# Optimization experiments

Measured on AMD Instinct MI355X. Metric: run time of the kernel, lower is better.

The kernel has to match this reference:

```python
import jax, jax.numpy as jnp
import numpy as np

B, S, D = 2, 2048, 2048
QH, KVH, HD = 32, 8, 64
GRP = QH // KVH  # GQA group size = 4


def setup_inputs() -> dict:
    key = jax.random.key(0)
    ks = jax.random.split(key, 9)
    x = jax.random.normal(ks[0], (B, S, D), jnp.float32)
    # RoPE angle table: [S, HD//2] -> stacked (cos, sin) -> [S, HD//2, 2]
    inv_freq = 1.0 / (10000.0 ** (np.arange(0, HD, 2, dtype=np.float32) / HD))
    ang = np.arange(S, dtype=np.float32)[:, None] * inv_freq[None, :]
    freqs = jnp.stack([jnp.cos(jnp.asarray(ang)), jnp.sin(jnp.asarray(ang))], axis=-1).astype(jnp.float32)
    w = 0.02
    Wq = jax.random.normal(ks[1], (D, QH * HD), jnp.float32) * w
    bq = jnp.zeros((QH * HD,), jnp.float32)
    Wk = jax.random.normal(ks[2], (D, KVH * HD), jnp.float32) * w
    bk = jnp.zeros((KVH * HD,), jnp.float32)
    Wv = jax.random.normal(ks[3], (D, KVH * HD), jnp.float32) * w
    bv = jnp.zeros((KVH * HD,), jnp.float32)
    Wo = jax.random.normal(ks[4], (QH * HD, D), jnp.float32) * w
    bo = jnp.zeros((D,), jnp.float32)
    return {"x": x, "freqs": freqs, "Wq": Wq, "bq": bq, "Wk": Wk, "bk": bk,
            "Wv": Wv, "bv": bv, "Wo": Wo, "bo": bo}


def _rope(xh, cos, sin):
    # xh: [b, s, h, hd]; complex rotation on adjacent pairs, like view_as_complex
    b, s, h, hd = xh.shape
    xp = xh.reshape(b, s, h, hd // 2, 2)
    x0, x1 = xp[..., 0], xp[..., 1]
    o0 = x0 * cos - x1 * sin
    o1 = x0 * sin + x1 * cos
    return jnp.stack([o0, o1], axis=-1).reshape(b, s, h, hd)


def reference(x, freqs, Wq, bq, Wk, bk, Wv, bv, Wo, bo):
    b, s, _ = x.shape
    q = (x @ Wq + bq).reshape(b, s, QH, HD)
    k = (x @ Wk + bk).reshape(b, s, KVH, HD)
    v = (x @ Wv + bv).reshape(b, s, KVH, HD)
    cos = freqs[:s, :, 0][None, :, None, :]  # [1, s, 1, hd//2]
    sin = freqs[:s, :, 1][None, :, None, :]
    q = _rope(q, cos, sin)
    k = _rope(k, cos, sin)
    # [b, h, s, hd]
    q = q.transpose(0, 2, 1, 3).reshape(b, KVH, GRP, s, HD)
    k = k.transpose(0, 2, 1, 3)  # [b, kvh, s, hd]
    v = v.transpose(0, 2, 1, 3)
    scores = jnp.einsum('bkgsh,bkth->bkgst', q, k) / jnp.sqrt(jnp.float32(HD))
    attn = jax.nn.softmax(scores, axis=-1)
    o = jnp.einsum('bkgst,bkth->bkgsh', attn, v)  # [b, kvh, grp, s, hd]
    o = o.reshape(b, QH, s, HD).transpose(0, 2, 1, 3).reshape(b, s, QH * HD)
    return o @ Wo + bo
```

## Files before the change

### kernel.cpp

```cpp
#include <hip/hip_runtime.h>
#include <stdint.h>

#define B_   2
#define S_   2048
#define D_   2048
#define QH_  32
#define KVH_ 8
#define HD_  64

typedef short  short8  __attribute__((ext_vector_type(8)));
typedef float  floatx4 __attribute__((ext_vector_type(4)));

__device__ __forceinline__ ushort f2b(float f) {
  union { float f; uint32_t u; } c; c.f = f;
  uint32_t u = c.u;
  return (ushort)((u + 0x7FFFu + ((u >> 16) & 1u)) >> 16);
}

__device__ __forceinline__ uint32_t fbits(float f) {
  union { float f; uint32_t u; } c; c.f = f;
  return c.u;
}

__device__ __forceinline__ short8 mk8(uint32_t a, uint32_t b, uint32_t c, uint32_t d) {
  union { uint4 u; short8 s; } v; v.u = (uint4){a, b, c, d}; return v.s;
}

__device__ __forceinline__ uint32_t cvtpk(float a, float b) {
  uint32_t r;
  asm("v_cvt_pk_bf16_f32 %0, %1, %2" : "=v"(r) : "v"(a), "v"(b));
  return r;
}

__device__ __forceinline__ void dma16(const void* g, void* l) {
  __builtin_amdgcn_global_load_lds(
      (const __attribute__((address_space(1))) uint32_t*)(uintptr_t)g,
      (__attribute__((address_space(3))) uint32_t*)(uintptr_t)l, 16, 0, 0);
}

#define QSCALE 0.18033688f


__global__ __launch_bounds__(256) void conv_x_kernel(const float* __restrict__ X,
                                                     ushort* __restrict__ Xb) {
  size_t i = ((size_t)blockIdx.x * 256 + threadIdx.x) * 4;
  float4 v = *(const float4*)(X + i);
  ushort4 o;
  o.x = f2b(v.x); o.y = f2b(v.y); o.z = f2b(v.z); o.w = f2b(v.w);
  *(ushort4*)(Xb + i) = o;
}

__global__ void tconv_all_kernel(const float* __restrict__ Wq, const float* __restrict__ Wk,
                                 const float* __restrict__ Wv, const float* __restrict__ Wo,
                                 ushort* __restrict__ wqkv, ushort* __restrict__ wo) {
  __shared__ float tile[32][33];
  int z = blockIdx.z;
  const float* W; ushort* Wt; int N;
  if (z == 0)      { W = Wq; Wt = wqkv;                        N = 2048; }
  else if (z == 1) { W = Wk; Wt = wqkv + (size_t)2048 * 2048;  N = 512;  }
  else if (z == 2) { W = Wv; Wt = wqkv + (size_t)2560 * 2048;  N = 512;  }
  else             { W = Wo; Wt = wo;                          N = 2048; }
  int bx = blockIdx.x, by = blockIdx.y;
  if (bx * 32 >= N) return;
  int tx = threadIdx.x, ty = threadIdx.y;
#pragma unroll
  for (int i = 0; i < 32; i += 8)
    tile[ty + i][tx] = W[(size_t)(by * 32 + ty + i) * N + bx * 32 + tx];
  __syncthreads();
#pragma unroll
  for (int i = 0; i < 32; i += 8)
    Wt[(size_t)(bx * 32 + ty + i) * 2048 + by * 32 + tx] = f2b(tile[tx][ty + i]);
}


__global__ __launch_bounds__(512, 2) void gemm_qkv_kernel(
    const ushort* __restrict__ A, const ushort* __restrict__ Bt,
    const float* __restrict__ bq, const float* __restrict__ bk,
    const float* __restrict__ bv, const float2* __restrict__ F2,
    ushort* __restrict__ qb, ushort* __restrict__ kb, ushort* __restrict__ vt) {
  __shared__ ushort sA[2][256 * 64];
  __shared__ ushort sB[2][256 * 64];
  const int tid  = threadIdx.x;
  const int bm   = blockIdx.y, bn = blockIdx.x;
  const int wave = tid >> 6, lane = tid & 63;
  const int quad = lane >> 4, l16 = lane & 15;
  const int wm2  = wave >> 2, wn4 = wave & 3;
  const int sw7  = l16 & 7;
  const int dr   = lane >> 3, du = (lane & 7) ^ dr;
  const int srow = wave * 8 + dr;
  const int lcol = (lane & 7) * 8;

  const ushort* Ab = A  + (size_t)(bm * 256) * 2048;
  const ushort* Bb = Bt + (size_t)(bn * 256) * 2048;

  floatx4 acc[8][4];
#pragma unroll
  for (int i = 0; i < 8; i++)
#pragma unroll
    for (int j = 0; j < 4; j++) acc[i][j] = (floatx4){0.f, 0.f, 0.f, 0.f};

  short8 af[4][2], bf[4][2];

#define STG_A(t, h) do {                                                      \
    dma16(Ab + (size_t)((h)*128 +      srow) * 2048 + (size_t)(t)*64 + du*8,  \
          &sA[(t)&1][((h)*128 +      srow) * 64 + lcol]);                     \
    dma16(Ab + (size_t)((h)*128 + 64 + srow) * 2048 + (size_t)(t)*64 + du*8,  \
          &sA[(t)&1][((h)*128 + 64 + srow) * 64 + lcol]);                     \
  } while (0)

#define STG_B(t, h) do {                                                      \
    dma16(Bb + (size_t)((h)*128 +      srow) * 2048 + (size_t)(t)*64 + du*8,  \
          &sB[(t)&1][((h)*128 +      srow) * 64 + lcol]);                     \
    dma16(Bb + (size_t)((h)*128 + 64 + srow) * 2048 + (size_t)(t)*64 + du*8,  \
          &sB[(t)&1][((h)*128 + 64 + srow) * 64 + lcol]);                     \
  } while (0)

#define LDA(Sb, mh) do {                                                      \
    _Pragma("unroll") for (int mi2 = 0; mi2 < 4; mi2++) {                     \
      const int rr = ((mh)*128 + wm2*64 + mi2*16 + l16) * 64;                 \
      af[mi2][0] = *(const short8*)&(Sb)[rr + (((quad    ) ^ sw7) * 8)];      \
      af[mi2][1] = *(const short8*)&(Sb)[rr + (((quad + 4) ^ sw7) * 8)];      \
    } } while (0)

#define LDB(Sb, nh) do {                                                      \
    _Pragma("unroll") for (int ni2 = 0; ni2 < 2; ni2++) {                     \
      const int rr = ((nh)*128 + wn4*32 + ni2*16 + l16) * 64;                 \
      bf[(nh)*2+ni2][0] = *(const short8*)&(Sb)[rr + (((quad    ) ^ sw7) * 8)]; \
      bf[(nh)*2+ni2][1] = *(const short8*)&(Sb)[rr + (((quad + 4) ^ sw7) * 8)]; \
    } } while (0)

#define MFMA_PH(mh, nh) do {                                                  \
    __builtin_amdgcn_s_setprio(1);                                           \
    _Pragma("unroll") for (int mi2 = 0; mi2 < 4; mi2++)                       \
    _Pragma("unroll") for (int ni2 = 0; ni2 < 2; ni2++)                       \
    _Pragma("unroll") for (int ks = 0; ks < 2; ks++)                          \
      acc[(mh)*4+mi2][(nh)*2+ni2] = __builtin_amdgcn_mfma_f32_16x16x32_bf16(  \
        af[mi2][ks], bf[(nh)*2+ni2][ks], acc[(mh)*4+mi2][(nh)*2+ni2], 0,0,0); \
    __builtin_amdgcn_s_setprio(0);                                            \
  } while (0)

#define PH_SYNC() do {                                                        \
    __builtin_amdgcn_sched_barrier(0);                                        \
    __builtin_amdgcn_s_barrier();                                             \
    asm volatile("s_waitcnt lgkmcnt(0)" ::: "memory");                        \
    __builtin_amdgcn_sched_barrier(0);                                        \
  } while (0)

#define PH_END() do {                                                         \
    __builtin_amdgcn_sched_barrier(0);                                        \
    __builtin_amdgcn_s_barrier();                                             \
    __builtin_amdgcn_sched_barrier(0);                                        \
  } while (0)

  STG_A(0, 0); STG_A(0, 1); STG_B(0, 0); STG_B(0, 1);
  STG_A(1, 0); STG_B(1, 0); STG_B(1, 1);
  asm volatile("s_waitcnt vmcnt(6)" ::: "memory");
  __builtin_amdgcn_s_barrier();

#pragma unroll 1
  for (int i = 0; i < 16; ++i) {
    const int t0 = 2 * i, t1 = 2 * i + 1;
    const bool more = (i < 15);
    const ushort* A0 = sA[0]; const ushort* B0 = sB[0];
    const ushort* A1 = sA[1]; const ushort* B1 = sB[1];

    LDB(B0, 0); LDA(A0, 0);
    STG_A(t1, 1);
    PH_SYNC(); MFMA_PH(0, 0); PH_END();

    LDB(B0, 1);
    if (more) STG_A(t0 + 2, 0);
    PH_SYNC(); MFMA_PH(0, 1); PH_END();

    LDA(A0, 1);
    if (more) STG_B(t0 + 2, 0);
    PH_SYNC(); MFMA_PH(1, 0); PH_END();

    if (more) STG_B(t0 + 2, 1);
    PH_SYNC(); MFMA_PH(1, 1);
    if (more) asm volatile("s_waitcnt vmcnt(6)" ::: "memory");
    else      asm volatile("s_waitcnt vmcnt(0)" ::: "memory");
    PH_END();

    LDB(B1, 0); LDA(A1, 0);
    if (more) STG_A(t0 + 2, 1);
    PH_SYNC(); MFMA_PH(0, 0); PH_END();

    LDB(B1, 1);
    if (more) STG_A(t1 + 2, 0);
    PH_SYNC(); MFMA_PH(0, 1); PH_END();

    LDA(A1, 1);
    if (more) STG_B(t1 + 2, 0);
    PH_SYNC(); MFMA_PH(1, 0); PH_END();

    if (more) STG_B(t1 + 2, 1);
    PH_SYNC(); MFMA_PH(1, 1);
    if (more) asm volatile("s_waitcnt vmcnt(6)" ::: "memory");
    PH_END();
  }

#undef STG_A
#undef STG_B
#undef LDA
#undef LDB
#undef MFMA_PH
#undef PH_SYNC
#undef PH_END

  const int isQ = (bn < 8);
  const int isV = (bn >= 10);
  const float sySign = (l16 & 1) ? 1.f : -1.f;

  const float* bsrc = isQ ? bq : (isV ? bv : bk);
  const int    boff = isQ ? 0  : (isV ? 2560 : 2048);

  float bvv[4];
#pragma unroll
  for (int ni = 0; ni < 4; ni++)
    bvv[ni] = bsrc[bn * 256 + (ni >> 1) * 128 + wn4 * 32 + (ni & 1) * 16 + l16 - boff];

  if (!isV) {
    ushort* dst = isQ ? qb : kb;
    const int NH   = isQ ? QH_ : KVH_;
    const int hoff = isQ ? 0 : 8;
    const int dpb  = l16 * 4 + (wn4 & 1) * 2;
#pragma unroll
    for (int mi = 0; mi < 8; mi++) {
#pragma unroll
      for (int r = 0; r < 4; r++) {
        int row = bm * 256 + (mi >> 2) * 128 + wm2 * 64 + (mi & 3) * 16 + quad * 4 + r;
        int s = row & 2047, bb = row >> 11;
        float o[4];
#pragma unroll
        for (int ni = 0; ni < 4; ni++) {
          float xv = acc[mi][ni][r] + bvv[ni];
          float2 cs = F2[s * 32 + (wn4 & 1) * 16 + (ni & 1) * 8 + (l16 >> 1)];
          float pp = __shfl_xor(xv, 1);
          float oo = fmaf(pp * sySign, cs.y, xv * cs.x);
          if (isQ) oo *= QSCALE;
          o[ni] = oo;
        }
#pragma unroll
        for (int hh = 0; hh < 2; hh++) {
          int h = (bn - hoff) * 4 + hh * 2 + (wn4 >> 1);
          size_t base = (((size_t)bb * NH + h) * S_ + s) * HD_ + dpb;
          ushort2 st; st.x = f2b(o[hh * 2 + 0]); st.y = f2b(o[hh * 2 + 1]);
          *(ushort2*)&dst[base] = st;
        }
      }
    }
  } else {
#pragma unroll
    for (int mi = 0; mi < 8; mi++) {
      int row0 = bm * 256 + (mi >> 2) * 128 + wm2 * 64 + (mi & 3) * 16 + quad * 4;
      int bb   = row0 >> 11;
      int posb = ((row0 & 2047) & ~63) + (mi & 2) * 16 + quad * 8 + (mi & 1) * 4;
#pragma unroll
      for (int ni = 0; ni < 4; ni++) {
        int h  = (bn - 10) * 4 + (ni >> 1) * 2 + (wn4 >> 1);
        int dt = (wn4 & 1) * 32 + (ni & 1) * 16 + l16;
        ushort4 st;
        st.x = f2b(acc[mi][ni][0] + bvv[ni]);
        st.y = f2b(acc[mi][ni][1] + bvv[ni]);
        st.z = f2b(acc[mi][ni][2] + bvv[ni]);
        st.w = f2b(acc[mi][ni][3] + bvv[ni]);
        *(ushort4*)&vt[(((size_t)bb * 8 + h) * 64 + dt) * (size_t)S_ + posb] = st;
      }
    }
  }
}


__global__ __launch_bounds__(256) void gemm_bt_kernel(
    const ushort* __restrict__ A, const ushort* __restrict__ Bt,
    const float* __restrict__ bias, float* __restrict__ C,
    int M, int N, int K) {
  __shared__ ushort sA[2][128 * 32];
  __shared__ ushort sB[2][128 * 32];
  const int tid  = threadIdx.x;
  const int bm   = blockIdx.y, bn = blockIdx.x;
  const int wave = tid >> 6, lane = tid & 63;
  const int quad = lane >> 4, l16 = lane & 15;
  const int wm   = (wave >> 1) * 64, wn = (wave & 1) * 64;

  const ushort* Ab = A  + (size_t)(bm * 128) * K;
  const ushort* Bb = Bt + (size_t)(bn * 128) * K;

  const int gr = lane >> 2;
  const int gu = (lane & 3) * 8;

  floatx4 acc[4][4];
#pragma unroll
  for (int i = 0; i < 4; i++)
#pragma unroll
    for (int j = 0; j < 4; j++) acc[i][j] = (floatx4){0.f, 0.f, 0.f, 0.f};

#pragma unroll
  for (int j = 0; j < 2; j++) {
    int row = j * 64 + wave * 16 + gr;
    dma16(Ab + (size_t)row * K + gu, &sA[0][j * 2048 + wave * 512]);
    dma16(Bb + (size_t)row * K + gu, &sB[0][j * 2048 + wave * 512]);
  }

  int cur = 0;
  for (int k0 = 0; k0 < K; k0 += 32) {
    __syncthreads();
    if (k0 + 32 < K) {
      int nxt = cur ^ 1;
#pragma unroll
      for (int j = 0; j < 2; j++) {
        int row = j * 64 + wave * 16 + gr;
        dma16(Ab + (size_t)row * K + k0 + 32 + gu, &sA[nxt][j * 2048 + wave * 512]);
        dma16(Bb + (size_t)row * K + k0 + 32 + gu, &sB[nxt][j * 2048 + wave * 512]);
      }
    }
    short8 af[4], bf[4];
#pragma unroll
    for (int mi = 0; mi < 4; mi++)
      af[mi] = *(const short8*)&sA[cur][(wm + mi * 16 + l16) * 32 + quad * 8];
#pragma unroll
    for (int ni = 0; ni < 4; ni++)
      bf[ni] = *(const short8*)&sB[cur][(wn + ni * 16 + l16) * 32 + quad * 8];
#pragma unroll
    for (int mi = 0; mi < 4; mi++)
#pragma unroll
      for (int ni = 0; ni < 4; ni++)
        acc[mi][ni] = __builtin_amdgcn_mfma_f32_16x16x32_bf16(
            af[mi], bf[ni], acc[mi][ni], 0, 0, 0);
    cur ^= 1;
  }

#pragma unroll
  for (int mi = 0; mi < 4; mi++) {
#pragma unroll
    for (int ni = 0; ni < 4; ni++) {
      int col  = bn * 128 + wn + ni * 16 + l16;
      float bv = bias[col];
#pragma unroll
      for (int r = 0; r < 4; r++) {
        int row = bm * 128 + wm + mi * 16 + quad * 4 + r;
        C[(size_t)row * N + col] = acc[mi][ni][r] + bv;
      }
    }
  }
}


__global__ __launch_bounds__(512, 4) void attn_kernel(
    const ushort* __restrict__ Q, const ushort* __restrict__ K,
    const ushort* __restrict__ Vt, ushort* __restrict__ O) {
  const int id  = blockIdx.x + 8 * (blockIdx.y + 32 * blockIdx.z);
  const int kvh = id & 7;
  const int qt  = (id >> 3) & 7;
  const int qh  = kvh * 4 + ((id >> 6) & 3);
  const int b   = id >> 8;
  const int tid = threadIdx.x;
  const int wave = tid >> 6, lane = tid & 63;
  const int quad = lane >> 4, l16 = lane & 15;

  __shared__ ushort kBuf[2][64 * 64];
  __shared__ ushort vBuf[2][64 * 64];

  const ushort* Qh = Q  + ((size_t)(b * QH_ + qh)) * S_ * HD_;
  const ushort* Kh = K  + ((size_t)(b * KVH_ + kvh)) * S_ * HD_;
  const ushort* Vh = Vt + ((size_t)(b * KVH_ + kvh)) * HD_ * S_;

  const int dr = lane >> 3;
  const int du = (lane & 7) ^ (dr & 7);
  const size_t kLaneOff = (size_t)(wave * 8 + dr) * 64 + du * 8;
  const size_t vLaneOff = (size_t)(wave * 8 + dr) * S_ + du * 8;
  const int swz = l16 & 7;

  const int q0 = qt * 256 + wave * 32;
  short8 aq[2][2];
#pragma unroll
  for (int m = 0; m < 2; m++)
#pragma unroll
    for (int s2 = 0; s2 < 2; s2++)
      aq[m][s2] = *(const short8*)(Qh + (size_t)(q0 + m * 16 + l16) * HD_ + s2 * 32 + quad * 8);

  floatx4 oacc[2][4];
#pragma unroll
  for (int m = 0; m < 2; m++)
#pragma unroll
    for (int t = 0; t < 4; t++) oacc[m][t] = (floatx4){0.f, 0.f, 0.f, 0.f};
  float ls[2] = {0.f, 0.f};

  dma16(Kh + kLaneOff, &kBuf[0][wave * 512]);
  dma16(Vh + vLaneOff, &vBuf[0][wave * 512]);

  int cur = 0;
  for (int kv0 = 0; kv0 < S_; kv0 += 64) {
    __syncthreads();
    if (kv0 + 64 < S_) {
      int nxt = cur ^ 1;
      dma16(Kh + (size_t)(kv0 + 64) * 64 + kLaneOff, &kBuf[nxt][wave * 512]);
      dma16(Vh + (size_t)(kv0 + 64) + vLaneOff,      &vBuf[nxt][wave * 512]);
    }

#pragma unroll
    for (int u = 0; u < 2; u++) {
      uint32_t pk[2][4];
#pragma unroll
      for (int cc = 0; cc < 2; cc++) {
        const int c = u * 2 + cc;
        short8 kf0 = *(const short8*)&kBuf[cur][(c * 16 + l16) * 64 + ((quad ^ swz) * 8)];
        short8 kf1 = *(const short8*)&kBuf[cur][(c * 16 + l16) * 64 + (((4 + quad) ^ swz) * 8)];
#pragma unroll
        for (int m = 0; m < 2; m++) {
          floatx4 sc = (floatx4){0.f, 0.f, 0.f, 0.f};
          __builtin_amdgcn_s_setprio(1);
          sc = __builtin_amdgcn_mfma_f32_16x16x32_bf16(kf0, aq[m][0], sc, 0, 0, 0);
          sc = __builtin_amdgcn_mfma_f32_16x16x32_bf16(kf1, aq[m][1], sc, 0, 0, 0);
          __builtin_amdgcn_s_setprio(0);
          float p0 = __builtin_amdgcn_exp2f(sc[0]);
          float p1 = __builtin_amdgcn_exp2f(sc[1]);
          float p2 = __builtin_amdgcn_exp2f(sc[2]);
          float p3 = __builtin_amdgcn_exp2f(sc[3]);
          ls[m] += (p0 + p1) + (p2 + p3);
          pk[m][cc * 2 + 0] = cvtpk(p0, p1);
          pk[m][cc * 2 + 1] = cvtpk(p2, p3);
        }
      }
#pragma unroll
      for (int t = 0; t < 4; t++) {
        const int row = (t * 16 + l16) * 64;
        short8 vf = *(const short8*)&vBuf[cur][row + (((u * 4 + quad) ^ swz) * 8)];
        __builtin_amdgcn_s_setprio(1);
#pragma unroll
        for (int m = 0; m < 2; m++) {
          short8 ap = mk8(pk[m][0], pk[m][1], pk[m][2], pk[m][3]);
          oacc[m][t] = __builtin_amdgcn_mfma_f32_16x16x32_bf16(ap, vf, oacc[m][t], 0, 0, 0);
        }
        __builtin_amdgcn_s_setprio(0);
      }
    }
    cur ^= 1;
  }

#pragma unroll
  for (int m = 0; m < 2; m++) {
    ls[m] += __shfl_xor(ls[m], 16);
    ls[m] += __shfl_xor(ls[m], 32);
  }
#pragma unroll
  for (int m = 0; m < 2; m++) {
#pragma unroll
    for (int r = 0; r < 4; r++) {
      float l = __shfl(ls[m], (lane & 48) | (quad * 4 + r));
      float inv = 1.0f / l;
      int srow = q0 + m * 16 + quad * 4 + r;
      size_t base = ((size_t)b * S_ + srow) * (QH_ * HD_) + (size_t)qh * HD_;
#pragma unroll
      for (int t = 0; t < 4; t++)
        O[base + t * 16 + l16] = f2b(oacc[m][t][r] * inv);
    }
  }
}


extern "C" void kernel_launch(void* const* d_in, const int* in_sizes, int n_in,
                              void* d_out, int out_size, void* d_ws, size_t ws_size,
                              hipStream_t stream) {
  const float* x  = (const float*)d_in[0];
  const float* fr = (const float*)d_in[1];
  const float* Wq = (const float*)d_in[2];
  const float* bq = (const float*)d_in[3];
  const float* Wk = (const float*)d_in[4];
  const float* bk = (const float*)d_in[5];
  const float* Wv = (const float*)d_in[6];
  const float* bv = (const float*)d_in[7];
  const float* Wo = (const float*)d_in[8];
  const float* bo = (const float*)d_in[9];
  float* out = (float*)d_out;
  char* ws = (char*)d_ws;

  ushort* xb    = (ushort*)(ws + 0);
  ushort* wqkv  = (ushort*)(ws + 16777216);
  ushort* wo    = (ushort*)(ws + 29360128);
  ushort* qb    = (ushort*)(ws + 37761024);
  ushort* kb    = (ushort*)(ws + 54538240);
  ushort* vt    = (ushort*)(ws + 62926848);
  ushort* ob    = xb;

  conv_x_kernel<<<8192, 256, 0, stream>>>(x, xb);
  tconv_all_kernel<<<dim3(64, 64, 4), dim3(32, 8), 0, stream>>>(Wq, Wk, Wv, Wo, wqkv, wo);

  gemm_qkv_kernel<<<dim3(3072 / 256, 4096 / 256), 512, 0, stream>>>(
      xb, wqkv, bq, bk, bv, (const float2*)fr, qb, kb, vt);

  attn_kernel<<<dim3(8, 32, 2), 512, 0, stream>>>(qb, kb, vt, ob);

  gemm_bt_kernel<<<dim3(2048 / 128, 4096 / 128), 256, 0, stream>>>(
      ob, wo, bo, out, 4096, 2048, 2048);
}
```

Before: 296.3 us.

## Triple-buffer K/V tiles in attention with explicit vmcnt waits

Moves the attention kernel's K/V shared-memory staging from double to triple buffering, prefetching two tiles ahead. Each iteration waits with an explicit s_waitcnt vmcnt(2) and a raw s_barrier instead of __syncthreads, so one tile's loads can stay in flight while the current tile is computed. The last tile is peeled out of the loop. This raises LDS use per block, which may reduce occupancy, and correctness now depends on the manual counter waits matching the number of outstanding DMA ops.

```diff
diff --git a/kernel.cpp b/kernel.cpp
--- a/kernel.cpp
+++ b/kernel.cpp
@@ -359,8 +359,8 @@
   const int wave = tid >> 6, lane = tid & 63;
   const int quad = lane >> 4, l16 = lane & 15;
 
-  __shared__ ushort kBuf[2][64 * 64];
-  __shared__ ushort vBuf[2][64 * 64];
+  __shared__ ushort kBuf[3][64 * 64];
+  __shared__ ushort vBuf[3][64 * 64];
 
   const ushort* Qh = Q  + ((size_t)(b * QH_ + qh)) * S_ * HD_;
   const ushort* Kh = K  + ((size_t)(b * KVH_ + kvh)) * S_ * HD_;
@@ -389,55 +389,75 @@
 
   dma16(Kh + kLaneOff, &kBuf[0][wave * 512]);
   dma16(Vh + vLaneOff, &vBuf[0][wave * 512]);
-
-  int cur = 0;
-  for (int kv0 = 0; kv0 < S_; kv0 += 64) {
-    __syncthreads();
-    if (kv0 + 64 < S_) {
-      int nxt = cur ^ 1;
-      dma16(Kh + (size_t)(kv0 + 64) * 64 + kLaneOff, &kBuf[nxt][wave * 512]);
-      dma16(Vh + (size_t)(kv0 + 64) + vLaneOff,      &vBuf[nxt][wave * 512]);
+  dma16(Kh + (size_t)64 * 64 + kLaneOff, &kBuf[1][wave * 512]);
+  dma16(Vh + 64 + vLaneOff,              &vBuf[1][wave * 512]);
+
+#define ATTN_TILE(KB, VB)                                                     \
+  do {                                                                        \
+    _Pragma("unroll")                                                         \
+    for (int u = 0; u < 2; u++) {                                             \
+      uint32_t pk[2][4];                                                      \
+      _Pragma("unroll")                                                       \
+      for (int cc = 0; cc < 2; cc++) {                                        \
+        const int c = u * 2 + cc;                                             \
+        short8 kf0 = *(const short8*)&(KB)[(c * 16 + l16) * 64 + ((quad ^ swz) * 8)];        \
+        short8 kf1 = *(const short8*)&(KB)[(c * 16 + l16) * 64 + (((4 + quad) ^ swz) * 8)];  \
+        _Pragma("unroll")                                                     \
+        for (int m = 0; m < 2; m++) {                                         \
+          floatx4 sc = (floatx4){0.f, 0.f, 0.f, 0.f};                         \
+          __builtin_amdgcn_s_setprio(1);                                      \
+          sc = __builtin_amdgcn_mfma_f32_16x16x32_bf16(kf0, aq[m][0], sc, 0, 0, 0); \
+          sc = __builtin_amdgcn_mfma_f32_16x16x32_bf16(kf1, aq[m][1], sc, 0, 0, 0); \
+          __builtin_amdgcn_s_setprio(0);                                      \
+          float p0 = __builtin_amdgcn_exp2f(sc[0]);                           \
+          float p1 = __builtin_amdgcn_exp2f(sc[1]);                           \
+          float p2 = __builtin_amdgcn_exp2f(sc[2]);                           \
+          float p3 = __builtin_amdgcn_exp2f(sc[3]);                           \
+          ls[m] += (p0 + p1) + (p2 + p3);                                     \
+          pk[m][cc * 2 + 0] = cvtpk(p0, p1);                                  \
+          pk[m][cc * 2 + 1] = cvtpk(p2, p3);                                  \
+        }                                                                     \
+      }                                                                       \
+      _Pragma("unroll")                                                       \
+      for (int t = 0; t < 4; t++) {                                           \
+        const int row = (t * 16 + l16) * 64;                                  \
+        short8 vf = *(const short8*)&(VB)[row + (((u * 4 + quad) ^ swz) * 8)]; \
+        __builtin_amdgcn_s_setprio(1);                                        \
+        _Pragma("unroll")                                                     \
+        for (int m = 0; m < 2; m++) {                                         \
+          short8 ap = mk8(pk[m][0], pk[m][1], pk[m][2], pk[m][3]);            \
+          oacc[m][t] = __builtin_amdgcn_mfma_f32_16x16x32_bf16(ap, vf, oacc[m][t], 0, 0, 0); \
+        }                                                                     \
+        __builtin_amdgcn_s_setprio(0);                                        \
+      }                                                                       \
+    }                                                                         \
+  } while (0)
+
+  int cur = 0, stg = 2;
+#pragma unroll 1
+  for (int i = 0; i < 31; ++i) {
+    __builtin_amdgcn_sched_barrier(0);
+    asm volatile("s_waitcnt vmcnt(2)" ::: "memory");
+    __builtin_amdgcn_s_barrier();
+    __builtin_amdgcn_sched_barrier(0);
+
+    if (i <= 29) {
+      size_t kv2 = (size_t)(i + 2) * 64;
+      dma16(Kh + kv2 * 64 + kLaneOff, &kBuf[stg][wave * 512]);
+      dma16(Vh + kv2 + vLaneOff,      &vBuf[stg][wave * 512]);
+      stg = (stg == 2) ? 0 : stg + 1;
     }
 
-#pragma unroll
-    for (int u = 0; u < 2; u++) {
-      uint32_t pk[2][4];
-#pragma unroll
-      for (int cc = 0; cc < 2; cc++) {
-        const int c = u * 2 + cc;
-        short8 kf0 = *(const short8*)&kBuf[cur][(c * 16 + l16) * 64 + ((quad ^ swz) * 8)];
-        short8 kf1 = *(const short8*)&kBuf[cur][(c * 16 + l16) * 64 + (((4 + quad) ^ swz) * 8)];
-#pragma unroll
-        for (int m = 0; m < 2; m++) {
-          floatx4 sc = (floatx4){0.f, 0.f, 0.f, 0.f};
-          __builtin_amdgcn_s_setprio(1);
-          sc = __builtin_amdgcn_mfma_f32_16x16x32_bf16(kf0, aq[m][0], sc, 0, 0, 0);
-          sc = __builtin_amdgcn_mfma_f32_16x16x32_bf16(kf1, aq[m][1], sc, 0, 0, 0);
-          __builtin_amdgcn_s_setprio(0);
-          float p0 = __builtin_amdgcn_exp2f(sc[0]);
-          float p1 = __builtin_amdgcn_exp2f(sc[1]);
-          float p2 = __builtin_amdgcn_exp2f(sc[2]);
-          float p3 = __builtin_amdgcn_exp2f(sc[3]);
-          ls[m] += (p0 + p1) + (p2 + p3);
-          pk[m][cc * 2 + 0] = cvtpk(p0, p1);
-          pk[m][cc * 2 + 1] = cvtpk(p2, p3);
-        }
-      }
-#pragma unroll
-      for (int t = 0; t < 4; t++) {
-        const int row = (t * 16 + l16) * 64;
-        short8 vf = *(const short8*)&vBuf[cur][row + (((u * 4 + quad) ^ swz) * 8)];
-        __builtin_amdgcn_s_setprio(1);
-#pragma unroll
-        for (int m = 0; m < 2; m++) {
-          short8 ap = mk8(pk[m][0], pk[m][1], pk[m][2], pk[m][3]);
-          oacc[m][t] = __builtin_amdgcn_mfma_f32_16x16x32_bf16(ap, vf, oacc[m][t], 0, 0, 0);
-        }
-        __builtin_amdgcn_s_setprio(0);
-      }
-    }
-    cur ^= 1;
-  }
+    ATTN_TILE(kBuf[cur], vBuf[cur]);
+    cur = (cur == 2) ? 0 : cur + 1;
+  }
+  __builtin_amdgcn_sched_barrier(0);
+  asm volatile("s_waitcnt vmcnt(0)" ::: "memory");
+  __builtin_amdgcn_s_barrier();
+  __builtin_amdgcn_sched_barrier(0);
+  ATTN_TILE(kBuf[cur], vBuf[cur]);
+
+#undef ATTN_TILE
 
 #pragma unroll
   for (int m = 0; m < 2; m++) {
```

Measured after the change: 302.6 us. 1.02x slower.
